# Kernel optimization log

Hardware: AMD Instinct MI355X
Metric: run time of the kernel (lower is better)

## Reference

```python
import jax, jax.numpy as jnp
import numpy as np
from jax import lax

BN_EPS = 1e-5

def conv2d(x, w, stride=1, pad=0, dil=1):
    return lax.conv_general_dilated(x, w, (stride, stride), [(pad, pad), (pad, pad)],
                                    rhs_dilation=(dil, dil),
                                    dimension_numbers=('NCHW', 'OIHW', 'NCHW'))

def bilinear_sample(x, py, px):
    # x: [B,C,H,W]; py,px: [B,K,H,W] absolute fractional coords -> [B,C,K,H,W]
    B, C, H, W = x.shape
    xf = x.reshape(B, C, H * W)
    y0 = jnp.floor(py); x0 = jnp.floor(px)
    ty = py - y0; tx = px - x0
    out = jnp.zeros((B, C) + py.shape[1:], x.dtype)
    for oy, wy in ((y0, 1.0 - ty), (y0 + 1.0, ty)):
        for ox, wx in ((x0, 1.0 - tx), (x0 + 1.0, tx)):
            valid = (oy >= 0) & (oy < H) & (ox >= 0) & (ox < W)
            yc = jnp.clip(oy, 0, H - 1).astype(jnp.int32)
            xc = jnp.clip(ox, 0, W - 1).astype(jnp.int32)
            idx = (yc * W + xc).reshape(B, -1)
            v = jax.vmap(lambda a, i: a[:, i])(xf, idx).reshape(B, C, *py.shape[1:])
            out = out + v * ((wy * wx) * valid.astype(x.dtype))[:, None]
    return out

def deform_dw(x, off_w, off_b, dw_w, k, pad, dil):
    # depthwise (groups=C) deformable conv2d, offset_groups=1, offsets interleaved (dy,dx)
    B, C, H, W = x.shape
    K = k * k
    off = conv2d(x, off_w, pad=pad, dil=dil) + off_b[None, :, None, None]
    off = off.reshape(B, K, 2, H, W)
    dy, dx = off[:, :, 0], off[:, :, 1]
    base = -pad + jnp.arange(k, dtype=x.dtype) * dil  # [k]
    ky = jnp.repeat(base, k); kx = jnp.tile(base, k)  # [K] row-major kernel taps
    py = jnp.arange(H, dtype=x.dtype)[None, None, :, None] + ky[None, :, None, None] + dy
    px = jnp.arange(W, dtype=x.dtype)[None, None, None, :] + kx[None, :, None, None] + dx
    s = bilinear_sample(x, py, px)  # [B,C,K,H,W]
    return jnp.einsum('bckhw,ck->bchw', s, dw_w)


def setup_inputs() -> dict:
    key = jax.random.key(0)
    ks = iter(jax.random.split(key, 40))
    B, C, H, W = 4, 128, 80, 80
    ch = C // 2
    def n(shape, scale=1.0):
        return jax.random.normal(next(ks), shape, jnp.float32) * scale
    inp = {'x': n((B, C, H, W))}
    inp['cv1_w'] = n((C, C, 3, 3), 0.05)
    inp['bn_g'] = jax.random.uniform(next(ks), (C,), jnp.float32, 0.5, 1.5)
    inp['bn_b'] = n((C,), 0.1)
    inp['bn_m'] = n((C,), 0.1)
    inp['bn_v'] = jax.random.uniform(next(ks), (C,), jnp.float32, 0.5, 1.5)
    # branch A: cv0 (3x3 pad1) -> cv_spatial (5x5 dil3 pad6); branch B: conv0 (5x5 pad2) -> conv_spatial (7x7 dil3 pad9)
    for name, k in (('a0', 3), ('a1', 5), ('b0', 5), ('b1', 7)):
        K = k * k
        inp[name + '_off_w'] = n((2 * K, ch, k, k), 0.02)
        inp[name + '_off_b'] = n((2 * K,), 0.02)
        inp[name + '_w'] = n((ch, K), 0.2)
    inp['conv1_w'] = n((ch, ch, 1, 1), 0.1)
    inp['conv1_b'] = n((ch,), 0.1)
    inp['conv2_w'] = n((ch, ch, 1, 1), 0.1)
    inp['conv2_b'] = n((ch,), 0.1)
    return inp


def reference(x, cv1_w, bn_g, bn_b, bn_m, bn_v,
              a0_off_w, a0_off_b, a0_w, a1_off_w, a1_off_b, a1_w,
              b0_off_w, b0_off_b, b0_w, b1_off_w, b1_off_b, b1_w,
              conv1_w, conv1_b, conv2_w, conv2_b):
    # cv1: Conv 3x3 + BN (inference form) + SiLU
    h = conv2d(x, cv1_w, pad=1)
    scale = (bn_g / jnp.sqrt(bn_v + BN_EPS))[None, :, None, None]
    h = (h - bn_m[None, :, None, None]) * scale + bn_b[None, :, None, None]
    h = jax.nn.silu(h)
    # deformable_LKA
    u = h
    y0, y1 = jnp.split(h, 2, axis=1)
    a = deform_dw(y0, a0_off_w, a0_off_b, a0_w, 3, 1, 1)
    a = deform_dw(a, a1_off_w, a1_off_b, a1_w, 5, 6, 3)
    a = conv2d(a, conv1_w) + conv1_b[None, :, None, None]
    b = deform_dw(y1, b0_off_w, b0_off_b, b0_w, 5, 2, 1)
    b = deform_dw(b, b1_off_w, b1_off_b, b1_w, 7, 9, 3)
    b = conv2d(b, conv2_w) + conv2_b[None, :, None, None]
    attn = jnp.concatenate([a, b], axis=1)
    return x + u * attn  # shortcut (c1 == c2, e=1.0)
```

## Files before the change

### kernel.cpp

```cpp
#include <hip/hip_runtime.h>

#define HH 80
#define WW 80
#define BB 4
#define NPIX (BB*HH*WW)
#define AS1 __attribute__((address_space(1)))
#define AS3 __attribute__((address_space(3)))

typedef _Float16 f16;
typedef _Float16 f16x8 __attribute__((ext_vector_type(8)));
typedef float    f32x4 __attribute__((ext_vector_type(4)));
typedef unsigned int uint;
typedef unsigned short ushort;

__device__ inline f16x8 splat8(uint u) {
    uint4 q = {u, u, u, u};
    return __builtin_bit_cast(f16x8, q);
}
__device__ inline ushort h_bits(float w) {
    f16 h = (f16)w;
    return __builtin_bit_cast(ushort, h);
}
__device__ inline int swiz200(int m)  { return (m & 7) * 25  + (m >> 3); }
__device__ inline int swiz1600(int m) { return (m & 7) * 200 + (m >> 3); }

struct PrepDesc {
    const float* src; f16* dst;
    int cout, cin, kk2, nt_tot, total, mode;
};
struct PrepArgs { PrepDesc d[11]; int grand_total; };

__global__ void prep_k(PrepArgs P) {
    for (int idx = blockIdx.x * 256 + threadIdx.x; idx < P.grand_total;
         idx += gridDim.x * 256) {
        int i = 0, base = 0;
        while (idx >= base + P.d[i].total) { base += P.d[i].total; i++; }
        const PrepDesc& D = P.d[i];
        int e = idx - base;
        if (D.mode == 0) {
            int j  = e & 7;
            int l  = (e >> 3) & 63;
            int rr = e >> 9;
            int ct = rr % D.nt_tot;
            int ks = rr / D.nt_tot;
            int kkk = ks * 32 + (l >> 4) * 8 + j;
            int tap = kkk / D.cin;
            int ci  = kkk % D.cin;
            int n = ct * 16 + (l & 15);
            float v = (n < D.cout) ? D.src[((size_t)n * D.cin + ci) * D.kk2 + tap] : 0.f;
            D.dst[e] = (f16)v;
        } else {
            int o = e & 63, tt = e >> 6;
            D.dst[e] = (f16)D.src[o * D.kk2 + tt];
        }
    }
}

__global__ void xcvt_k(const float* __restrict__ x, f16* __restrict__ xb) {
    __shared__ float l[128 * 17];
    int t = threadIdx.x;
    int blk = blockIdx.x;
    int wb = blk % 5;
    int r  = blk / 5;
    int h  = r % HH;
    int b  = r / HH;
    int w0 = wb * 16;
    size_t pixbase = (size_t)(b * HH + h) * WW + w0;
    for (int e = t; e < 2048; e += 256) {
        int c = e >> 4, p = e & 15;
        l[c * 17 + p] = x[((size_t)(b * 128 + c)) * (HH * WW) + h * WW + w0 + p];
    }
    __syncthreads();
    for (int e = t; e < 2048; e += 256) {
        int c = e & 127, p = e >> 7;
        xb[(pixbase + p) * 128 + c] = (f16)l[c * 17 + p];
    }
}

struct MArgs {
    const f16* in; const f16* wp; const float* bias;
    float* outf; f16* outh;
    const float* bn_g; const float* bn_b; const float* bn_m; const float* bn_v;
    const f16* zbuf;
    int cin_tot, ci_base, nt_tot, cout, out_stride, pad, dil;
};

template<int K, int CIN, int NT, bool OUT_F16, bool BNSILU>
__device__ __forceinline__ void mconv_body(int bx, int by, char* lds, const MArgs& A) {
    constexpr int NST  = K * K * CIN / 64;
    constexpr int AF16 = 8192;
    constexpr int BF16 = NT * 1024;
    f16* Al = (f16*)lds;
    f16* Bl = (f16*)(lds + 2 * AF16 * 2);
    const int t    = threadIdx.x;
    const int lane = t & 63;
    const int wv   = t >> 6;
    const int blkpix = bx * 128;
    const int ntb    = by * NT;

    auto stage = [&](int s, int buf) {
        int tap, ch0;
        if constexpr (CIN == 64) { tap = s; ch0 = 0; }
        else                     { tap = s >> 1; ch0 = (s & 1) * 64; }
        int ky = tap / K, kx = tap - ky * K;
        int g    = t & 7;
        int prel = t >> 3;
#pragma unroll
        for (int i = 0; i < 4; i++) {
            int pl  = prel + i * 32;
            int pix = blkpix + pl;
            int b   = pix / 6400;
            int rem = pix - b * 6400;
            int h = rem / WW, w = rem - h * WW;
            int y = h + ky * A.dil - A.pad;
            int x = w + kx * A.dil - A.pad;
            bool v = ((unsigned)y < (unsigned)HH) & ((unsigned)x < (unsigned)WW);
            int sg = g ^ (pl & 7);
            const f16* src = v
                ? A.in + ((size_t)(b * 6400 + y * WW + x)) * A.cin_tot + A.ci_base + ch0 + sg * 8
                : A.zbuf + sg * 8;
            __builtin_amdgcn_global_load_lds((const AS1 void*)src,
                (AS3 void*)(Al + buf * AF16 + i * 2048 + t * 8), 16, 0, 0);
        }
        if constexpr (NT == 4) {
#pragma unroll
            for (int j = 0; j < 2; j++) {
                const f16* src = A.wp + ((size_t)(2 * s + j) * A.nt_tot + ntb) * 512 + t * 8;
                __builtin_amdgcn_global_load_lds((const AS1 void*)src,
                    (AS3 void*)(Bl + buf * BF16 + j * 2048 + t * 8), 16, 0, 0);
            }
        } else {
            const f16* src = A.wp + (size_t)(2 * s) * A.nt_tot * 512 + t * 8;
            __builtin_amdgcn_global_load_lds((const AS1 void*)src,
                (AS3 void*)(Bl + buf * BF16 + t * 8), 16, 0, 0);
        }
    };

    f32x4 acc[2][NT];
#pragma unroll
    for (int m = 0; m < 2; m++)
#pragma unroll
        for (int n = 0; n < NT; n++) acc[m][n] = (f32x4){0.f, 0.f, 0.f, 0.f};

    auto compute = [&](int buf) {
#pragma unroll
        for (int j = 0; j < 2; j++) {
            f16x8 bfr[NT];
#pragma unroll
            for (int n = 0; n < NT; n++)
                bfr[n] = *(const f16x8*)(Bl + buf * BF16 + j * NT * 512 + n * 512 + lane * 8);
#pragma unroll
            for (int m = 0; m < 2; m++) {
                int px = wv * 32 + m * 16 + (lane & 15);
                int gi = (j * 4 + (lane >> 4)) ^ (px & 7);
                f16x8 a = *(const f16x8*)(Al + buf * AF16 + px * 64 + gi * 8);
#pragma unroll
                for (int n = 0; n < NT; n++)
                    acc[m][n] = __builtin_amdgcn_mfma_f32_16x16x32_f16(a, bfr[n], acc[m][n], 0, 0, 0);
            }
        }
    };

    stage(0, 0);
    __syncthreads();
    for (int s = 0; s < NST; s++) {
        int buf = s & 1;
        if (s + 1 < NST) stage(s + 1, buf ^ 1);
        compute(buf);
        __syncthreads();
    }

    const int nloc = lane & 15;
#pragma unroll
    for (int m = 0; m < 2; m++) {
        const int prow = blkpix + wv * 32 + m * 16 + (lane >> 4) * 4;
#pragma unroll
        for (int ct = 0; ct < NT; ct++) {
            int n = (ntb + ct) * 16 + nloc;
            if (n >= A.cout) continue;
            float sc = 1.f, sh = 0.f, bv = 0.f;
            if (BNSILU) {
                sc = A.bn_g[n] / sqrtf(A.bn_v[n] + 1e-5f);
                sh = A.bn_b[n] - A.bn_m[n] * sc;
            } else if (A.bias) {
                bv = A.bias[n];
            }
#pragma unroll
            for (int r = 0; r < 4; r++) {
                float vv = acc[m][ct][r] + bv;
                if (BNSILU) { vv = vv * sc + sh; vv = vv / (1.f + expf(-vv)); }
                size_t o = (size_t)(prow + r) * A.out_stride + n;
                if (OUT_F16) A.outh[o] = (f16)vv; else A.outf[o] = vv;
            }
        }
    }
}

__global__ __launch_bounds__(256, 3) void mconv_main_k(MArgs A) {
    __shared__ char lds[2 * 16384 + 2 * 8192];
    int b = blockIdx.x;
    mconv_body<3, 128, 4, true, true>(swiz200(b % 200), b / 200, lds, A);
}

template<int K1, int C1, int N1, int K2, int C2, int N2>
__global__ __launch_bounds__(256, 3) void mconv_pair_k(MArgs A1, int nblk1, MArgs A2) {
    constexpr int MAXNT = (N1 > N2) ? N1 : N2;
    __shared__ char lds[2 * 16384 + 2 * MAXNT * 2048];
    int b = blockIdx.x;
    if (b < nblk1) {
        mconv_body<K1, C1, N1, false, false>(swiz200(b % 200), b / 200, lds, A1);
    } else {
        int bb = b - nblk1;
        mconv_body<K2, C2, N2, false, false>(swiz200(bb % 200), bb / 200, lds, A2);
    }
}

struct DArgs {
    const f16* in; const float* off; const f16* dwh; f16* out;
    int csh, ci_base, off_stride;
};
struct alignas(16) DEnt { int o00; short dx1, dy1; uint w01, w23; };

template<int KS, int PAD, int DIL>
__device__ __forceinline__ void dsample_body(int blk, char* ldsraw, const DArgs A) {
    constexpr int K = KS * KS;
    DEnt* ent = (DEnt*)ldsraw;
    const int t = threadIdx.x;

    for (int e = t; e < 16 * K; e += 128) {
        int p  = e / K;
        int kk = e - p * K;
        int pix = blk * 16 + p;
        int b   = pix / (HH * WW);
        int rem = pix - b * (HH * WW);
        int h   = rem / WW;
        int w   = rem - h * WW;
        int ky = kk / KS, kx = kk - ky * KS;
        float2 d = *(const float2*)&A.off[(size_t)pix * A.off_stride + 2 * kk];
        float py = (float)(h + ky * DIL - PAD) + d.x;
        float px = (float)(w + kx * DIL - PAD) + d.y;
        float y0f = floorf(py), x0f = floorf(px);
        float ty = py - y0f, tx = px - x0f;
        int iy0 = (int)y0f, ix0 = (int)x0f;
        bool vy0 = (unsigned)iy0 < (unsigned)HH;
        bool vy1 = (unsigned)(iy0 + 1) < (unsigned)HH;
        bool vx0 = (unsigned)ix0 < (unsigned)WW;
        bool vx1 = (unsigned)(ix0 + 1) < (unsigned)WW;
        int cy0 = min(max(iy0, 0), HH - 1), cy1 = min(max(iy0 + 1, 0), HH - 1);
        int cx0 = min(max(ix0, 0), WW - 1), cx1 = min(max(ix0 + 1, 0), WW - 1);
        float wy0 = 1.f - ty, wx0 = 1.f - tx;
        ushort w00 = h_bits(wy0 * wx0 * ((vy0 && vx0) ? 1.f : 0.f));
        ushort w01 = h_bits(wy0 * tx  * ((vy0 && vx1) ? 1.f : 0.f));
        ushort w10 = h_bits(ty  * wx0 * ((vy1 && vx0) ? 1.f : 0.f));
        ushort w11 = h_bits(ty  * tx  * ((vy1 && vx1) ? 1.f : 0.f));
        DEnt E;
        E.o00 = (b * (HH * WW) + cy0 * WW + cx0) << A.csh;
        E.dx1 = (short)((cx1 - cx0) << A.csh);
        E.dy1 = (short)(((cy1 - cy0) * WW) << A.csh);
        E.w01 = (uint)w00 | ((uint)w01 << 16);
        E.w23 = (uint)w10 | ((uint)w11 << 16);
        ent[e] = E;
    }
    __syncthreads();

    const int li  = t & 7;
    const int p   = t >> 3;
    const int ch0 = li * 8;
    const int pix = blk * 16 + p;
    const char* ibase = (const char*)(A.in + A.ci_base) + ch0 * 2;
    const f16*  dwb  = A.dwh + ch0;

    float acc[8];
#pragma unroll
    for (int j = 0; j < 8; j++) acc[j] = 0.f;

#pragma unroll 4
    for (int kk = 0; kk < K; kk++) {
        DEnt e = ent[p * K + kk];
        uint s00 = (e.w01 & 0xffffu) * 0x10001u;
        uint s01 = (e.w01 >> 16)     * 0x10001u;
        uint s10 = (e.w23 & 0xffffu) * 0x10001u;
        uint s11 = (e.w23 >> 16)     * 0x10001u;
        int o00 = e.o00, o01 = o00 + e.dx1, o10 = o00 + e.dy1, o11 = o10 + e.dx1;
        f16x8 c00 = *(const f16x8*)(ibase + o00);
        f16x8 c01 = *(const f16x8*)(ibase + o01);
        f16x8 c10 = *(const f16x8*)(ibase + o10);
        f16x8 c11 = *(const f16x8*)(ibase + o11);
        f16x8 s = c00 * splat8(s00);
        s = c01 * splat8(s01) + s;
        s = c10 * splat8(s10) + s;
        s = c11 * splat8(s11) + s;
        f16x8 dw = *(const f16x8*)(dwb + kk * 64);
#pragma unroll
        for (int j = 0; j < 8; j++)
            acc[j] = fmaf((float)dw[j], (float)s[j], acc[j]);
    }

    f16x8 o;
#pragma unroll
    for (int j = 0; j < 8; j++) o[j] = (f16)acc[j];
    *(f16x8*)&A.out[(size_t)pix * 64 + ch0] = o;
}

template<int K1, int P1, int D1, int K2, int P2, int D2>
__global__ __launch_bounds__(128, 4) void dsample_pair_k(DArgs A1, int nblk1, DArgs A2) {
    constexpr int KMAX = (K1 * K1 > K2 * K2) ? K1 * K1 : K2 * K2;
    __shared__ char lds[16 * KMAX * 16];
    int b = blockIdx.x;
    if (b < nblk1) dsample_body<K1, P1, D1>(swiz1600(b), lds, A1);
    else           dsample_body<K2, P2, D2>(swiz1600(b - nblk1), lds, A2);
}

__global__ void final_k(const float* __restrict__ x, const f16* __restrict__ u,
                        const float* __restrict__ af, const float* __restrict__ bf,
                        float* __restrict__ out) {
    __shared__ float lu[16 * 130];
    __shared__ float lat[16 * 130];
    int t   = threadIdx.x;
    int blk = blockIdx.x;
    int wb = blk % 5;
    int r  = blk / 5;
    int h  = r % HH;
    int b  = r / HH;
    int w0 = wb * 16;
    size_t pixbase = (size_t)(b * HH + h) * WW + w0;
    for (int e = t; e < 16 * 128; e += 256) {
        int c = e & 127;
        int p = e >> 7;
        lu[p * 130 + c]  = (float)u[(pixbase + p) * 128 + c];
        lat[p * 130 + c] = (c < 64) ? af[(pixbase + p) * 64 + c]
                                    : bf[(pixbase + p) * 64 + (c - 64)];
    }
    __syncthreads();
    for (int e = t; e < 16 * 128; e += 256) {
        int p = e & 15;
        int c = e >> 4;
        size_t gi = ((size_t)(b * 128 + c) * HH + h) * WW + w0 + p;
        out[gi] = x[gi] + lu[p * 130 + c] * lat[p * 130 + c];
    }
}

extern "C" void kernel_launch(void* const* d_in, const int* in_sizes, int n_in,
                              void* d_out, int out_size, void* d_ws, size_t ws_size,
                              hipStream_t stream) {
    const float* x        = (const float*)d_in[0];
    const float* cv1_w    = (const float*)d_in[1];
    const float* bn_g     = (const float*)d_in[2];
    const float* bn_b     = (const float*)d_in[3];
    const float* bn_m     = (const float*)d_in[4];
    const float* bn_v     = (const float*)d_in[5];
    const float* a0_off_w = (const float*)d_in[6];
    const float* a0_off_b = (const float*)d_in[7];
    const float* a0_w     = (const float*)d_in[8];
    const float* a1_off_w = (const float*)d_in[9];
    const float* a1_off_b = (const float*)d_in[10];
    const float* a1_w     = (const float*)d_in[11];
    const float* b0_off_w = (const float*)d_in[12];
    const float* b0_off_b = (const float*)d_in[13];
    const float* b0_w     = (const float*)d_in[14];
    const float* b1_off_w = (const float*)d_in[15];
    const float* b1_off_b = (const float*)d_in[16];
    const float* b1_w     = (const float*)d_in[17];
    const float* conv1_w  = (const float*)d_in[18];
    const float* conv1_b  = (const float*)d_in[19];
    const float* conv2_w  = (const float*)d_in[20];
    const float* conv2_b  = (const float*)d_in[21];
    float* out = (float*)d_out;

    char* wsb = (char*)d_ws;
    size_t pos = 0;
    auto alloc = [&](size_t bytes) -> void* {
        void* p = (void*)(wsb + pos);
        pos += (bytes + 255) & ~(size_t)255;
        return p;
    };
    f16*   zbuf   = (f16*)  alloc(256);
    f16*   xb     = (f16*)  alloc((size_t)NPIX * 128 * 2);
    f16*   u      = (f16*)  alloc((size_t)NPIX * 128 * 2);
    f16*   s0a    = (f16*)  alloc((size_t)NPIX * 64 * 2);
    f16*   s0b    = (f16*)  alloc((size_t)NPIX * 64 * 2);
    f16*   s1a    = (f16*)  alloc((size_t)NPIX * 64 * 2);
    f16*   s1b    = (f16*)  alloc((size_t)NPIX * 64 * 2);
    float* offa   = (float*)alloc((size_t)NPIX * 64 * 4);
    float* offb   = (float*)alloc((size_t)NPIX * 128 * 4);
    float* aF     = offa;
    float* bF     = offb;
    f16*   pcv1   = (f16*)  alloc((size_t)36 * 8 * 512 * 2);
    f16*   pa0    = (f16*)  alloc((size_t)18 * 2 * 512 * 2);
    f16*   pa1    = (f16*)  alloc((size_t)50 * 4 * 512 * 2);
    f16*   pb0    = (f16*)  alloc((size_t)50 * 4 * 512 * 2);
    f16*   pb1    = (f16*)  alloc((size_t)98 * 8 * 512 * 2);
    f16*   pc1    = (f16*)  alloc((size_t)2  * 4 * 512 * 2);
    f16*   pc2    = (f16*)  alloc((size_t)2  * 4 * 512 * 2);
    f16*   dwh_a0 = (f16*)  alloc(9  * 64 * 2);
    f16*   dwh_a1 = (f16*)  alloc(25 * 64 * 2);
    f16*   dwh_b0 = (f16*)  alloc(25 * 64 * 2);
    f16*   dwh_b1 = (f16*)  alloc(49 * 64 * 2);

    hipMemsetAsync(zbuf, 0, 256, stream);
    xcvt_k<<<dim3(BB * HH * 5), dim3(256), 0, stream>>>(x, xb);

    PrepArgs P;
    int gt = 0, di = 0;
    auto addpk = [&](const float* src, f16* dst, int cout, int cin, int kk2, int nt, int nk) {
        PrepDesc D; D.src = src; D.dst = dst; D.cout = cout; D.cin = cin; D.kk2 = kk2;
        D.nt_tot = nt; D.total = nk * nt * 512; D.mode = 0;
        P.d[di++] = D; gt += D.total;
    };
    auto addtw = [&](const float* src, f16* dst, int K) {
        PrepDesc D; D.src = src; D.dst = dst; D.cout = 64; D.cin = 64; D.kk2 = K;
        D.nt_tot = 1; D.total = K * 64; D.mode = 1;
        P.d[di++] = D; gt += D.total;
    };
    addpk(cv1_w,    pcv1, 128, 128, 9,  8, 36);
    addpk(a0_off_w, pa0,  18,  64,  9,  2, 18);
    addpk(a1_off_w, pa1,  50,  64,  25, 4, 50);
    addpk(b0_off_w, pb0,  50,  64,  25, 4, 50);
    addpk(b1_off_w, pb1,  98,  64,  49, 8, 98);
    addpk(conv1_w,  pc1,  64,  64,  1,  4, 2);
    addpk(conv2_w,  pc2,  64,  64,  1,  4, 2);
    addtw(a0_w, dwh_a0, 9);
    addtw(a1_w, dwh_a1, 25);
    addtw(b0_w, dwh_b0, 25);
    addtw(b1_w, dwh_b1, 49);
    P.grand_total = gt;
    prep_k<<<dim3(1024), dim3(256), 0, stream>>>(P);

    auto margs = [&](const f16* in, int cin_tot, int ci_base, const f16* wp, int nt_tot,
                     const float* bias, int cout, int out_stride, int pad, int dil,
                     float* outf, f16* outh) {
        MArgs A;
        A.in = in; A.wp = wp; A.bias = bias; A.outf = outf; A.outh = outh;
        A.bn_g = bn_g; A.bn_b = bn_b; A.bn_m = bn_m; A.bn_v = bn_v; A.zbuf = zbuf;
        A.cin_tot = cin_tot; A.ci_base = ci_base; A.nt_tot = nt_tot; A.cout = cout;
        A.out_stride = out_stride; A.pad = pad; A.dil = dil;
        return A;
    };
    auto dargs = [&](const f16* in, int csh, int ci_base, const float* off, int off_stride,
                     const f16* dwh, f16* outp) {
        DArgs A;
        A.in = in; A.off = off; A.dwh = dwh; A.out = outp;
        A.csh = csh; A.ci_base = ci_base; A.off_stride = off_stride;
        return A;
    };

    mconv_main_k<<<dim3(400), dim3(256), 0, stream>>>(
        margs(xb, 128, 0, pcv1, 8, nullptr, 128, 128, 1, 1, nullptr, u));

    mconv_pair_k<3, 64, 2, 5, 64, 4><<<dim3(400), dim3(256), 0, stream>>>(
        margs(u, 128, 0,  pa0, 2, a0_off_b, 18, 64, 1, 1, offa, nullptr), 200,
        margs(u, 128, 64, pb0, 4, b0_off_b, 50, 64, 2, 1, offb, nullptr));

    dsample_pair_k<3, 1, 1, 5, 2, 1><<<dim3(3200), dim3(128), 0, stream>>>(
        dargs(u, 8, 0,  offa, 64, dwh_a0, s0a), 1600,
        dargs(u, 8, 64, offb, 64, dwh_b0, s0b));

    mconv_pair_k<5, 64, 4, 7, 64, 4><<<dim3(600), dim3(256), 0, stream>>>(
        margs(s0a, 64, 0, pa1, 4, a1_off_b, 50, 64,  6, 3, offa, nullptr), 200,
        margs(s0b, 64, 0, pb1, 8, b1_off_b, 98, 128, 9, 3, offb, nullptr));

    dsample_pair_k<5, 6, 3, 7, 9, 3><<<dim3(3200), dim3(128), 0, stream>>>(
        dargs(s0a, 7, 0, offa, 64,  dwh_a1, s1a), 1600,
        dargs(s0b, 7, 0, offb, 128, dwh_b1, s1b));

    mconv_pair_k<1, 64, 4, 1, 64, 4><<<dim3(400), dim3(256), 0, stream>>>(
        margs(s1a, 64, 0, pc1, 4, conv1_b, 64, 64, 0, 1, aF, nullptr), 200,
        margs(s1b, 64, 0, pc2, 4, conv2_b, 64, 64, 0, 1, bF, nullptr));

    final_k<<<dim3(BB * HH * 5), dim3(256), 0, stream>>>(x, u, aF, bF, out);
}
```

Before: 195.1 us.

## Interleave paired-kernel block assignment and unroll deformable sampling loop by two

The paired conv and deformable-sample kernels now interleave blocks of the two sub-problems instead of running them as two contiguous ranges. The pair kernels use a ratio R, and the sample kernel uses odd and even block indices. This is meant to mix the light and heavy workloads across CUs so the tail is more balanced. The sampling inner loop is fully unrolled two taps at a time so eight gathers are in flight together, and the sample kernel's launch bound is raised to 6 blocks per SIMD. That raises register pressure and may cause spills.

```diff
diff --git a/kernel.cpp b/kernel.cpp
--- a/kernel.cpp
+++ b/kernel.cpp
@@ -202,16 +202,17 @@
     mconv_body<3, 128, 4, true, true>(swiz200(b % 200), b / 200, lds, A);
 }
 
-template<int K1, int C1, int N1, int K2, int C2, int N2>
-__global__ __launch_bounds__(256, 3) void mconv_pair_k(MArgs A1, int nblk1, MArgs A2) {
+template<int K1, int C1, int N1, int K2, int C2, int N2, int R>
+__global__ __launch_bounds__(256, 3) void mconv_pair_k(MArgs A1, MArgs A2) {
     constexpr int MAXNT = (N1 > N2) ? N1 : N2;
     __shared__ char lds[2 * 16384 + 2 * MAXNT * 2048];
     int b = blockIdx.x;
-    if (b < nblk1) {
-        mconv_body<K1, C1, N1, false, false>(swiz200(b % 200), b / 200, lds, A1);
+    int q = b / (R + 1), m = b - q * (R + 1);
+    if (m == R) {
+        mconv_body<K1, C1, N1, false, false>(swiz200(q % 200), q / 200, lds, A1);
     } else {
-        int bb = b - nblk1;
-        mconv_body<K2, C2, N2, false, false>(swiz200(bb % 200), bb / 200, lds, A2);
+        int idx = q * R + m;
+        mconv_body<K2, C2, N2, false, false>(swiz200(idx % 200), idx / 200, lds, A2);
     }
 }
 
@@ -268,32 +269,60 @@
     const int ch0 = li * 8;
     const int pix = blk * 16 + p;
     const char* ibase = (const char*)(A.in + A.ci_base) + ch0 * 2;
-    const f16*  dwb  = A.dwh + ch0;
+    const f16*  dwb   = A.dwh + ch0;
 
     float acc[8];
 #pragma unroll
     for (int j = 0; j < 8; j++) acc[j] = 0.f;
 
-#pragma unroll 4
-    for (int kk = 0; kk < K; kk++) {
-        DEnt e = ent[p * K + kk];
-        uint s00 = (e.w01 & 0xffffu) * 0x10001u;
-        uint s01 = (e.w01 >> 16)     * 0x10001u;
-        uint s10 = (e.w23 & 0xffffu) * 0x10001u;
-        uint s11 = (e.w23 >> 16)     * 0x10001u;
-        int o00 = e.o00, o01 = o00 + e.dx1, o10 = o00 + e.dy1, o11 = o10 + e.dx1;
-        f16x8 c00 = *(const f16x8*)(ibase + o00);
-        f16x8 c01 = *(const f16x8*)(ibase + o01);
-        f16x8 c10 = *(const f16x8*)(ibase + o10);
-        f16x8 c11 = *(const f16x8*)(ibase + o11);
-        f16x8 s = c00 * splat8(s00);
-        s = c01 * splat8(s01) + s;
-        s = c10 * splat8(s10) + s;
-        s = c11 * splat8(s11) + s;
-        f16x8 dw = *(const f16x8*)(dwb + kk * 64);
+#pragma unroll
+    for (int kk = 0; kk + 1 < K; kk += 2) {
+        DEnt e0 = ent[p * K + kk];
+        DEnt e1 = ent[p * K + kk + 1];
+        const char* a00 = ibase + e0.o00;
+        const char* a10 = a00 + e0.dy1;
+        const char* b00 = ibase + e1.o00;
+        const char* b10 = b00 + e1.dy1;
+        f16x8 c0 = *(const f16x8*)a00;
+        f16x8 c1 = *(const f16x8*)(a00 + e0.dx1);
+        f16x8 c2 = *(const f16x8*)a10;
+        f16x8 c3 = *(const f16x8*)(a10 + e0.dx1);
+        f16x8 c4 = *(const f16x8*)b00;
+        f16x8 c5 = *(const f16x8*)(b00 + e1.dx1);
+        f16x8 c6 = *(const f16x8*)b10;
+        f16x8 c7 = *(const f16x8*)(b10 + e1.dx1);
+        f16x8 dw0 = *(const f16x8*)(dwb + kk * 64);
+        f16x8 dw1 = *(const f16x8*)(dwb + (kk + 1) * 64);
+        f16x8 s0 = c0 * splat8((e0.w01 & 0xffffu) * 0x10001u);
+        s0 = c1 * splat8((e0.w01 >> 16)     * 0x10001u) + s0;
+        s0 = c2 * splat8((e0.w23 & 0xffffu) * 0x10001u) + s0;
+        s0 = c3 * splat8((e0.w23 >> 16)     * 0x10001u) + s0;
+        f16x8 s1 = c4 * splat8((e1.w01 & 0xffffu) * 0x10001u);
+        s1 = c5 * splat8((e1.w01 >> 16)     * 0x10001u) + s1;
+        s1 = c6 * splat8((e1.w23 & 0xffffu) * 0x10001u) + s1;
+        s1 = c7 * splat8((e1.w23 >> 16)     * 0x10001u) + s1;
+#pragma unroll
+        for (int j = 0; j < 8; j++) {
+            acc[j] = fmaf((float)dw0[j], (float)s0[j], acc[j]);
+            acc[j] = fmaf((float)dw1[j], (float)s1[j], acc[j]);
+        }
+    }
+    {
+        DEnt e0 = ent[p * K + K - 1];
+        const char* a00 = ibase + e0.o00;
+        const char* a10 = a00 + e0.dy1;
+        f16x8 c0 = *(const f16x8*)a00;
+        f16x8 c1 = *(const f16x8*)(a00 + e0.dx1);
+        f16x8 c2 = *(const f16x8*)a10;
+        f16x8 c3 = *(const f16x8*)(a10 + e0.dx1);
+        f16x8 dw0 = *(const f16x8*)(dwb + (K - 1) * 64);
+        f16x8 s0 = c0 * splat8((e0.w01 & 0xffffu) * 0x10001u);
+        s0 = c1 * splat8((e0.w01 >> 16)     * 0x10001u) + s0;
+        s0 = c2 * splat8((e0.w23 & 0xffffu) * 0x10001u) + s0;
+        s0 = c3 * splat8((e0.w23 >> 16)     * 0x10001u) + s0;
 #pragma unroll
         for (int j = 0; j < 8; j++)
-            acc[j] = fmaf((float)dw[j], (float)s[j], acc[j]);
+            acc[j] = fmaf((float)dw0[j], (float)s0[j], acc[j]);
     }
 
     f16x8 o;
@@ -303,12 +332,12 @@
 }
 
 template<int K1, int P1, int D1, int K2, int P2, int D2>
-__global__ __launch_bounds__(128, 4) void dsample_pair_k(DArgs A1, int nblk1, DArgs A2) {
+__global__ __launch_bounds__(128, 6) void dsample_pair_k(DArgs A1, DArgs A2) {
     constexpr int KMAX = (K1 * K1 > K2 * K2) ? K1 * K1 : K2 * K2;
     __shared__ char lds[16 * KMAX * 16];
     int b = blockIdx.x;
-    if (b < nblk1) dsample_body<K1, P1, D1>(swiz1600(b), lds, A1);
-    else           dsample_body<K2, P2, D2>(swiz1600(b - nblk1), lds, A2);
+    if (b & 1) dsample_body<K2, P2, D2>(swiz1600(b >> 1), lds, A2);
+    else       dsample_body<K1, P1, D1>(swiz1600(b >> 1), lds, A1);
 }
 
 __global__ void final_k(const float* __restrict__ x, const f16* __restrict__ u,
@@ -447,24 +476,24 @@
     mconv_main_k<<<dim3(400), dim3(256), 0, stream>>>(
         margs(xb, 128, 0, pcv1, 8, nullptr, 128, 128, 1, 1, nullptr, u));
 
-    mconv_pair_k<3, 64, 2, 5, 64, 4><<<dim3(400), dim3(256), 0, stream>>>(
-        margs(u, 128, 0,  pa0, 2, a0_off_b, 18, 64, 1, 1, offa, nullptr), 200,
+    mconv_pair_k<3, 64, 2, 5, 64, 4, 1><<<dim3(400), dim3(256), 0, stream>>>(
+        margs(u, 128, 0,  pa0, 2, a0_off_b, 18, 64, 1, 1, offa, nullptr),
         margs(u, 128, 64, pb0, 4, b0_off_b, 50, 64, 2, 1, offb, nullptr));
 
     dsample_pair_k<3, 1, 1, 5, 2, 1><<<dim3(3200), dim3(128), 0, stream>>>(
-        dargs(u, 8, 0,  offa, 64, dwh_a0, s0a), 1600,
+        dargs(u, 8, 0,  offa, 64, dwh_a0, s0a),
         dargs(u, 8, 64, offb, 64, dwh_b0, s0b));
 
-    mconv_pair_k<5, 64, 4, 7, 64, 4><<<dim3(600), dim3(256), 0, stream>>>(
-        margs(s0a, 64, 0, pa1, 4, a1_off_b, 50, 64,  6, 3, offa, nullptr), 200,
+    mconv_pair_k<5, 64, 4, 7, 64, 4, 2><<<dim3(600), dim3(256), 0, stream>>>(
+        margs(s0a, 64, 0, pa1, 4, a1_off_b, 50, 64,  6, 3, offa, nullptr),
         margs(s0b, 64, 0, pb1, 8, b1_off_b, 98, 128, 9, 3, offb, nullptr));
 
     dsample_pair_k<5, 6, 3, 7, 9, 3><<<dim3(3200), dim3(128), 0, stream>>>(
-        dargs(s0a, 7, 0, offa, 64,  dwh_a1, s1a), 1600,
+        dargs(s0a, 7, 0, offa, 64,  dwh_a1, s1a),
         dargs(s0b, 7, 0, offb, 128, dwh_b1, s1b));
 
-    mconv_pair_k<1, 64, 4, 1, 64, 4><<<dim3(400), dim3(256), 0, stream>>>(
-        margs(s1a, 64, 0, pc1, 4, conv1_b, 64, 64, 0, 1, aF, nullptr), 200,
+    mconv_pair_k<1, 64, 4, 1, 64, 4, 1><<<dim3(400), dim3(256), 0, stream>>>(
+        margs(s1a, 64, 0, pc1, 4, conv1_b, 64, 64, 0, 1, aF, nullptr),
         margs(s1b, 64, 0, pc2, 4, conv2_b, 64, 64, 0, 1, bF, nullptr));
 
     final_k<<<dim3(BB * HH * 5), dim3(256), 0, stream>>>(x, u, aF, bF, out);
```

New measurement: 386.7 us. 1.98x slower.
